# Kernel tuning notes

Measured on AMD Instinct MI355X. Metric: run time of the kernel, lower is better.

Reference implementation:

```python
import jax, jax.numpy as jnp
import numpy as np

N = 50000        # nodes
E = 800000       # edges (avg degree 16)
H = 128          # hidden_channels
R = 6            # num_radial
SH = 3           # spin_hidden_channels


def _linear_params(key, out_dim, in_dim):
    # torch Linear default init: U(-1/sqrt(in), 1/sqrt(in)) for weight and bias
    kw, kb = jax.random.split(key)
    bound = 1.0 / np.sqrt(in_dim)
    W = jax.random.uniform(kw, (out_dim, in_dim), minval=-bound, maxval=bound, dtype=jnp.float32)
    b = jax.random.uniform(kb, (out_dim,), minval=-bound, maxval=bound, dtype=jnp.float32)
    return W, b


def setup_inputs() -> dict:
    key = jax.random.key(0)
    ks = jax.random.split(key, 9)
    x = jax.random.randint(ks[0], (N,), 0, 95)                       # atom types
    s = jax.random.randint(ks[1], (N,), 0, 3)                        # spin class in {0,1,2} == (spin + 1)
    rbf = jax.random.normal(ks[2], (E, R), dtype=jnp.float32)
    i = jax.random.randint(ks[3], (E,), 0, N)
    j = jax.random.randint(ks[4], (E,), 0, N)
    emb_w = jax.random.uniform(ks[5], (95, H), minval=-np.sqrt(3), maxval=np.sqrt(3), dtype=jnp.float32)
    spin_w, spin_b = _linear_params(ks[6], SH, 3)
    rbf_w, rbf_b = _linear_params(ks[7], H, R)
    lin_w, lin_b = _linear_params(ks[8], H, 3 * H + 2 * SH)
    return {"x": x, "s": s, "rbf": rbf, "i": i, "j": j,
            "emb_w": emb_w, "spin_w": spin_w, "spin_b": spin_b,
            "rbf_w": rbf_w, "rbf_b": rbf_b, "lin_w": lin_w, "lin_b": lin_b}


def reference(x, s, rbf, i, j, emb_w, spin_w, spin_b, rbf_w, rbf_b, lin_w, lin_b):
    act = jax.nn.silu
    h = emb_w[x]                                              # [N, H] embedding lookup
    spin_oh = jax.nn.one_hot(s, 3, dtype=spin_w.dtype)        # [N, 3]
    spin_feat = spin_oh @ spin_w.T + spin_b                   # [N, SH]
    r = act(rbf @ rbf_w.T + rbf_b)                            # [E, H]
    # concat order matches torch: [x_i, spin_i, x_j, spin_j, rbf]
    feat = jnp.concatenate([h[i], spin_feat[i], h[j], spin_feat[j], r], axis=-1)  # [E, 3H+2SH]
    return act(feat @ lin_w.T + lin_b)                        # [E, H]
```

## Files before the change

### kernel.cpp

```cpp
#include <hip/hip_runtime.h>
#include <hip/hip_bf16.h>

#define NH   128
#define NR   6
#define NCOL 390
#define TILE_E 128
#define LDK  136
#define NBLK 512

typedef __attribute__((ext_vector_type(8))) short bf16x8;
typedef __attribute__((ext_vector_type(4))) float f32x4;

__device__ __forceinline__ float fast_silu(float v) {
    return v * __builtin_amdgcn_rcpf(1.0f + __expf(-v));
}

__global__ void prep_all(const float* __restrict__ emb_w,
                         const float* __restrict__ spin_w,
                         const float* __restrict__ spin_b,
                         const float* __restrict__ lin_w,
                         const float* __restrict__ lin_b,
                         float* __restrict__ Ci, float* __restrict__ Cj,
                         __hip_bfloat16* __restrict__ Wb) {
    int b = blockIdx.x;
    int tid = threadIdx.x;
    if (b >= 190) {
        int idx = (b - 190) * 128 + tid;
        int n = idx >> 7, k = idx & 127;
        Wb[idx] = __float2bfloat16(lin_w[(size_t)n * NCOL + 262 + k]);
        return;
    }
    int side = b & 1;
    int a    = b >> 1;
    int n    = tid;
    const int col0 = side ? 131 : 0;
    const int cols = side ? 259 : 128;
    const float* wrow = lin_w + (size_t)n * NCOL;
    const float* ew   = emb_w + a * NH;
    float dot = side ? 0.0f : lin_b[n];
    #pragma unroll 8
    for (int k = 0; k < NH; ++k)
        dot += ew[k] * wrow[col0 + k];
    float* dst = (side ? Cj : Ci) + (size_t)(a * 3) * NH + n;
    #pragma unroll
    for (int sc = 0; sc < 3; ++sc) {
        float acc = dot;
        #pragma unroll
        for (int c = 0; c < 3; ++c)
            acc += (spin_w[c * 3 + sc] + spin_b[c]) * wrow[cols + c];
        dst[(size_t)sc * NH] = acc;
    }
}

__global__ __launch_bounds__(512, 4) void fused_main(
        const int*   __restrict__ x,   const int* __restrict__ s,
        const float* __restrict__ rbf,
        const int*   __restrict__ gi,  const int* __restrict__ gj,
        const float* __restrict__ rbf_w, const float* __restrict__ rbf_b,
        const float* __restrict__ Ci,  const float* __restrict__ Cj,
        const __hip_bfloat16* __restrict__ Wb,
        float* __restrict__ out, int E, int ntiles) {
    __shared__ __align__(16) __hip_bfloat16 w_lds[NH * LDK];
    __shared__ __align__(16) __hip_bfloat16 r_lds[TILE_E * LDK];
    __shared__ int ci_lds[TILE_E], cj_lds[TILE_E];

    const int tid = threadIdx.x;

    int sci = 0, scj = 0;
    auto load_idx = [&](int tt) {
        const int en0 = tt * TILE_E;
        if (tid >= 384) {
            int e = en0 + (tid - 384); if (e >= E) e = E - 1;
            int ii = gi[e];
            sci = x[ii] * 3 + s[ii];
        }
        if (tid < 128) {
            int e = en0 + tid; if (e >= E) e = E - 1;
            int jj = gj[e];
            scj = x[jj] * 3 + s[jj];
        }
    };

    const int t0 = blockIdx.x;
    const int gstride = gridDim.x;
    load_idx(t0);

    {
        const uint4* src = (const uint4*)Wb;
        #pragma unroll
        for (int it = 0; it < 4; ++it) {
            int l = it * 512 + tid;
            uint4 v = src[l];
            *(uint4*)&w_lds[(l >> 4) * LDK + (l & 15) * 8] = v;
        }
    }

    const int kgrp = tid & 15;
    const int egrp = tid >> 4;
    float wr[8][6];
    float br[8];
    #pragma unroll
    for (int j = 0; j < 8; ++j) {
        int k = kgrp * 8 + j;
        #pragma unroll
        for (int i = 0; i < 6; ++i) wr[j][i] = rbf_w[k * NR + i];
        br[j] = rbf_b[k];
    }

    const int wave   = tid >> 6;
    const int lane   = tid & 63;
    const int lane15 = lane & 15;
    const int quad   = lane >> 4;
    const int e_sub  = wave * 16;
    const int e_row  = e_sub + quad * 4;

    for (int t = t0; t < ntiles; t += gstride) {
        const int e0t = t * TILE_E;
        __syncthreads();
        if (tid >= 384) ci_lds[tid - 384] = sci;
        if (tid < 128)  cj_lds[tid] = scj;

        {
            const int e4 = e0t + egrp * 4;
            float c[4][6];
            if (e4 + 4 <= E) {
                const float4* q = (const float4*)(rbf + (size_t)e4 * NR);
                float4 q0 = q[0], q1 = q[1], q2 = q[2], q3 = q[3], q4 = q[4], q5 = q[5];
                c[0][0]=q0.x; c[0][1]=q0.y; c[0][2]=q0.z; c[0][3]=q0.w; c[0][4]=q1.x; c[0][5]=q1.y;
                c[1][0]=q1.z; c[1][1]=q1.w; c[1][2]=q2.x; c[1][3]=q2.y; c[1][4]=q2.z; c[1][5]=q2.w;
                c[2][0]=q3.x; c[2][1]=q3.y; c[2][2]=q3.z; c[2][3]=q3.w; c[2][4]=q4.x; c[2][5]=q4.y;
                c[3][0]=q4.z; c[3][1]=q4.w; c[3][2]=q5.x; c[3][3]=q5.y; c[3][4]=q5.z; c[3][5]=q5.w;
            } else {
                #pragma unroll
                for (int r = 0; r < 4; ++r) {
                    int er = e4 + r; if (er > E - 1) er = E - 1;
                    const float* rp = rbf + (size_t)er * NR;
                    #pragma unroll
                    for (int i = 0; i < 6; ++i) c[r][i] = rp[i];
                }
            }
            #pragma unroll
            for (int r = 0; r < 4; ++r) {
                bf16x8 pk;
                #pragma unroll
                for (int j = 0; j < 8; ++j) {
                    float a = br[j] + c[r][0] * wr[j][0] + c[r][1] * wr[j][1]
                                    + c[r][2] * wr[j][2] + c[r][3] * wr[j][3]
                                    + c[r][4] * wr[j][4] + c[r][5] * wr[j][5];
                    __hip_bfloat16 h = __float2bfloat16(fast_silu(a));
                    pk[j] = *(short*)&h;
                }
                *(bf16x8*)&r_lds[(egrp * 4 + r) * LDK + kgrp * 8] = pk;
            }
        }
        __syncthreads();

        bf16x8 afrag[4];
        #pragma unroll
        for (int kt = 0; kt < 4; ++kt)
            afrag[kt] = *(const bf16x8*)&r_lds[(e_sub + lane15) * LDK + kt * 32 + quad * 8];

        const float* cip[4]; const float* cjp[4]; float* op[4];
        #pragma unroll
        for (int reg = 0; reg < 4; ++reg) {
            cip[reg] = Ci + ci_lds[e_row + reg] * NH + lane15;
            cjp[reg] = Cj + cj_lds[e_row + reg] * NH + lane15;
            op[reg]  = out + (size_t)(e0t + e_row + reg) * NH + lane15;
        }
        const bool tail = (e0t + TILE_E > E);

        int tn = t + gstride;
        if (tn < ntiles) load_idx(tn);

        #pragma unroll
        for (int nt = 0; nt < 8; ++nt) {
            f32x4 acc = {0.f, 0.f, 0.f, 0.f};
            #pragma unroll
            for (int kt = 0; kt < 4; ++kt) {
                bf16x8 bfrag = *(const bf16x8*)&w_lds[(nt * 16 + lane15) * LDK + kt * 32 + quad * 8];
                acc = __builtin_amdgcn_mfma_f32_16x16x32_bf16(afrag[kt], bfrag, acc, 0, 0, 0);
            }
            #pragma unroll
            for (int reg = 0; reg < 4; ++reg) {
                float base = cip[reg][nt * 16] + cjp[reg][nt * 16];
                float v = acc[reg] + base;
                float sv = fast_silu(v);
                if (!tail || (e0t + e_row + reg < E))
                    __builtin_nontemporal_store(sv, op[reg] + nt * 16);
            }
        }
    }
}

extern "C" void kernel_launch(void* const* d_in, const int* in_sizes, int n_in,
                              void* d_out, int out_size, void* d_ws, size_t ws_size,
                              hipStream_t stream) {
    const int*   x      = (const int*)  d_in[0];
    const int*   s      = (const int*)  d_in[1];
    const float* rbf    = (const float*)d_in[2];
    const int*   gi     = (const int*)  d_in[3];
    const int*   gj     = (const int*)  d_in[4];
    const float* emb_w  = (const float*)d_in[5];
    const float* spin_w = (const float*)d_in[6];
    const float* spin_b = (const float*)d_in[7];
    const float* rbf_w  = (const float*)d_in[8];
    const float* rbf_b  = (const float*)d_in[9];
    const float* lin_w  = (const float*)d_in[10];
    const float* lin_b  = (const float*)d_in[11];
    const int E = in_sizes[3];

    float* Ci = (float*)d_ws;
    float* Cj = Ci + 285 * NH;
    __hip_bfloat16* Wb = (__hip_bfloat16*)(Cj + 285 * NH);

    prep_all<<<318, 128, 0, stream>>>(emb_w, spin_w, spin_b, lin_w, lin_b, Ci, Cj, Wb);

    int ntiles = (E + TILE_E - 1) / TILE_E;
    int nblk = ntiles < NBLK ? ntiles : NBLK;
    fused_main<<<nblk, 512, 0, stream>>>(x, s, rbf, gi, gj, rbf_w, rbf_b,
                                         Ci, Cj, Wb, (float*)d_out, E, ntiles);
}
```

Baseline: 563.8 us.

## Make each wave self-contained: per-wave index gather, shuffles, no block barriers

Restructures the main loop so each wave computes the rbf activations only for its own 16 edges and gathers its own gi/gj-derived table indices, passing them between lanes with shuffles instead of through shared memory. This removes both per-tile __syncthreads, so waves no longer stall on each other. It also double-buffers the Ci/Cj gathers one n-tile ahead of the MFMA work. The cost is that the index loads are no longer prefetched a tile ahead, and relying on intra-wave ordering of LDS writes and reads with no barrier assumes the same wave does both.

```diff
diff --git a/kernel.cpp b/kernel.cpp
--- a/kernel.cpp
+++ b/kernel.cpp
@@ -62,118 +62,113 @@
         float* __restrict__ out, int E, int ntiles) {
     __shared__ __align__(16) __hip_bfloat16 w_lds[NH * LDK];
     __shared__ __align__(16) __hip_bfloat16 r_lds[TILE_E * LDK];
-    __shared__ int ci_lds[TILE_E], cj_lds[TILE_E];
-
-    const int tid = threadIdx.x;
-
-    int sci = 0, scj = 0;
-    auto load_idx = [&](int tt) {
-        const int en0 = tt * TILE_E;
-        if (tid >= 384) {
-            int e = en0 + (tid - 384); if (e >= E) e = E - 1;
-            int ii = gi[e];
-            sci = x[ii] * 3 + s[ii];
-        }
-        if (tid < 128) {
-            int e = en0 + tid; if (e >= E) e = E - 1;
-            int jj = gj[e];
-            scj = x[jj] * 3 + s[jj];
-        }
-    };
-
-    const int t0 = blockIdx.x;
-    const int gstride = gridDim.x;
-    load_idx(t0);
-
-    {
-        const uint4* src = (const uint4*)Wb;
-        #pragma unroll
-        for (int it = 0; it < 4; ++it) {
-            int l = it * 512 + tid;
-            uint4 v = src[l];
-            *(uint4*)&w_lds[(l >> 4) * LDK + (l & 15) * 8] = v;
-        }
-    }
-
-    const int kgrp = tid & 15;
-    const int egrp = tid >> 4;
-    float wr[8][6];
-    float br[8];
-    #pragma unroll
-    for (int j = 0; j < 8; ++j) {
-        int k = kgrp * 8 + j;
-        #pragma unroll
-        for (int i = 0; i < 6; ++i) wr[j][i] = rbf_w[k * NR + i];
-        br[j] = rbf_b[k];
-    }
-
+
+    const int tid    = threadIdx.x;
     const int wave   = tid >> 6;
     const int lane   = tid & 63;
     const int lane15 = lane & 15;
     const int quad   = lane >> 4;
     const int e_sub  = wave * 16;
-    const int e_row  = e_sub + quad * 4;
+
+    {
+        const uint4* src = (const uint4*)Wb;
+        #pragma unroll
+        for (int it = 0; it < 4; ++it) {
+            int l = it * 512 + tid;
+            uint4 v = src[l];
+            *(uint4*)&w_lds[(l >> 4) * LDK + (l & 15) * 8] = v;
+        }
+    }
+
+    float wr[8][6];
+    float br[8];
+    #pragma unroll
+    for (int j = 0; j < 8; ++j) {
+        int k = lane15 * 8 + j;
+        #pragma unroll
+        for (int i = 0; i < 6; ++i) wr[j][i] = rbf_w[k * NR + i];
+        br[j] = rbf_b[k];
+    }
+
+    __syncthreads();
+
+    const int t0 = blockIdx.x;
+    const int gstride = gridDim.x;
 
     for (int t = t0; t < ntiles; t += gstride) {
-        const int e0t = t * TILE_E;
-        __syncthreads();
-        if (tid >= 384) ci_lds[tid - 384] = sci;
-        if (tid < 128)  cj_lds[tid] = scj;
-
-        {
-            const int e4 = e0t + egrp * 4;
-            float c[4][6];
-            if (e4 + 4 <= E) {
-                const float4* q = (const float4*)(rbf + (size_t)e4 * NR);
-                float4 q0 = q[0], q1 = q[1], q2 = q[2], q3 = q[3], q4 = q[4], q5 = q[5];
-                c[0][0]=q0.x; c[0][1]=q0.y; c[0][2]=q0.z; c[0][3]=q0.w; c[0][4]=q1.x; c[0][5]=q1.y;
-                c[1][0]=q1.z; c[1][1]=q1.w; c[1][2]=q2.x; c[1][3]=q2.y; c[1][4]=q2.z; c[1][5]=q2.w;
-                c[2][0]=q3.x; c[2][1]=q3.y; c[2][2]=q3.z; c[2][3]=q3.w; c[2][4]=q4.x; c[2][5]=q4.y;
-                c[3][0]=q4.z; c[3][1]=q4.w; c[3][2]=q5.x; c[3][3]=q5.y; c[3][4]=q5.z; c[3][5]=q5.w;
-            } else {
+        const int ew0 = t * TILE_E + e_sub;
+
+        int civ = 0, cjv = 0;
+        if (lane < 16) {
+            int e = ew0 + lane; if (e > E - 1) e = E - 1;
+            int ii = gi[e], jj = gj[e];
+            civ = x[ii] * 3 + s[ii];
+            cjv = x[jj] * 3 + s[jj];
+        }
+
+        const int e4 = ew0 + quad * 4;
+        float c[4][6];
+        if (e4 + 4 <= E) {
+            const float4* q = (const float4*)(rbf + (size_t)e4 * NR);
+            float4 q0 = q[0], q1 = q[1], q2 = q[2], q3 = q[3], q4 = q[4], q5 = q[5];
+            c[0][0]=q0.x; c[0][1]=q0.y; c[0][2]=q0.z; c[0][3]=q0.w; c[0][4]=q1.x; c[0][5]=q1.y;
+            c[1][0]=q1.z; c[1][1]=q1.w; c[1][2]=q2.x; c[1][3]=q2.y; c[1][4]=q2.z; c[1][5]=q2.w;
+            c[2][0]=q3.x; c[2][1]=q3.y; c[2][2]=q3.z; c[2][3]=q3.w; c[2][4]=q4.x; c[2][5]=q4.y;
+            c[3][0]=q4.z; c[3][1]=q4.w; c[3][2]=q5.x; c[3][3]=q5.y; c[3][4]=q5.z; c[3][5]=q5.w;
+        } else {
+            #pragma unroll
+            for (int r = 0; r < 4; ++r) {
+                int er = e4 + r; if (er > E - 1) er = E - 1;
+                const float* rp = rbf + (size_t)er * NR;
                 #pragma unroll
-                for (int r = 0; r < 4; ++r) {
-                    int er = e4 + r; if (er > E - 1) er = E - 1;
-                    const float* rp = rbf + (size_t)er * NR;
-                    #pragma unroll
-                    for (int i = 0; i < 6; ++i) c[r][i] = rp[i];
-                }
-            }
-            #pragma unroll
-            for (int r = 0; r < 4; ++r) {
-                bf16x8 pk;
-                #pragma unroll
-                for (int j = 0; j < 8; ++j) {
-                    float a = br[j] + c[r][0] * wr[j][0] + c[r][1] * wr[j][1]
-                                    + c[r][2] * wr[j][2] + c[r][3] * wr[j][3]
-                                    + c[r][4] * wr[j][4] + c[r][5] * wr[j][5];
-                    __hip_bfloat16 h = __float2bfloat16(fast_silu(a));
-                    pk[j] = *(short*)&h;
-                }
-                *(bf16x8*)&r_lds[(egrp * 4 + r) * LDK + kgrp * 8] = pk;
-            }
-        }
-        __syncthreads();
+                for (int i = 0; i < 6; ++i) c[r][i] = rp[i];
+            }
+        }
+
+        #pragma unroll
+        for (int r = 0; r < 4; ++r) {
+            bf16x8 pk;
+            #pragma unroll
+            for (int j = 0; j < 8; ++j) {
+                float a = br[j] + c[r][0] * wr[j][0] + c[r][1] * wr[j][1]
+                                + c[r][2] * wr[j][2] + c[r][3] * wr[j][3]
+                                + c[r][4] * wr[j][4] + c[r][5] * wr[j][5];
+                __hip_bfloat16 h = __float2bfloat16(fast_silu(a));
+                pk[j] = *(short*)&h;
+            }
+            *(bf16x8*)&r_lds[(e_sub + quad * 4 + r) * LDK + lane15 * 8] = pk;
+        }
 
         bf16x8 afrag[4];
         #pragma unroll
         for (int kt = 0; kt < 4; ++kt)
             afrag[kt] = *(const bf16x8*)&r_lds[(e_sub + lane15) * LDK + kt * 32 + quad * 8];
 
-        const float* cip[4]; const float* cjp[4]; float* op[4];
+        int cio[4], cjo[4];
         #pragma unroll
         for (int reg = 0; reg < 4; ++reg) {
-            cip[reg] = Ci + ci_lds[e_row + reg] * NH + lane15;
-            cjp[reg] = Cj + cj_lds[e_row + reg] * NH + lane15;
-            op[reg]  = out + (size_t)(e0t + e_row + reg) * NH + lane15;
-        }
-        const bool tail = (e0t + TILE_E > E);
-
-        int tn = t + gstride;
-        if (tn < ntiles) load_idx(tn);
-
+            cio[reg] = __shfl(civ, quad * 4 + reg, 64) * NH + lane15;
+            cjo[reg] = __shfl(cjv, quad * 4 + reg, 64) * NH + lane15;
+        }
+        float* ob = out + (size_t)e4 * NH + lane15;
+        const bool full = (e4 + 4 <= E);
+
+        float ga[2][4], gb[2][4];
+        #pragma unroll
+        for (int reg = 0; reg < 4; ++reg) {
+            ga[0][reg] = Ci[cio[reg]];
+            gb[0][reg] = Cj[cjo[reg]];
+        }
         #pragma unroll
         for (int nt = 0; nt < 8; ++nt) {
+            const int cur = nt & 1, nxt = cur ^ 1;
+            if (nt < 7) {
+                #pragma unroll
+                for (int reg = 0; reg < 4; ++reg) {
+                    ga[nxt][reg] = Ci[cio[reg] + (nt + 1) * 16];
+                    gb[nxt][reg] = Cj[cjo[reg] + (nt + 1) * 16];
+                }
+            }
             f32x4 acc = {0.f, 0.f, 0.f, 0.f};
             #pragma unroll
             for (int kt = 0; kt < 4; ++kt) {
@@ -182,11 +177,10 @@
             }
             #pragma unroll
             for (int reg = 0; reg < 4; ++reg) {
-                float base = cip[reg][nt * 16] + cjp[reg][nt * 16];
-                float v = acc[reg] + base;
+                float v = acc[reg] + ga[cur][reg] + gb[cur][reg];
                 float sv = fast_silu(v);
-                if (!tail || (e0t + e_row + reg < E))
-                    __builtin_nontemporal_store(sv, op[reg] + nt * 16);
+                if (full || (e4 + reg < E))
+                    __builtin_nontemporal_store(sv, ob + reg * NH + nt * 16);
             }
         }
     }
```

Measured after the change: 744.2 us. 1.32x slower.
